# Kernel optimization log

Hardware: AMD Instinct MI355X
Metric: run time of the kernel (lower is better)

The kernel has to match this reference:

```python
import jax, jax.numpy as jnp
import numpy as np

N_NODES, D_H, D_MSG, N_LAYERS = 512, 64, 64, 3
T, E = 128, 8192


def setup_inputs() -> dict:
    key = jax.random.key(0)
    ks = jax.random.split(key, 16)
    s = 0.1
    t = jax.random.uniform(ks[0], (T,), dtype=jnp.float32)
    edge_index = jax.random.randint(ks[1], (2, E), 0, N_NODES, dtype=jnp.int64)
    inp = {
        "t": t,
        "edge_index": edge_index,
        "enc_w": jax.random.normal(ks[2], (1 + N_NODES, D_H), jnp.float32) * s,
        "enc_b": jnp.zeros((D_H,), jnp.float32),
        "msg1_w": jax.random.normal(ks[3], (N_LAYERS, 2 * D_H, D_MSG), jnp.float32) * s,
        "msg1_b": jnp.zeros((N_LAYERS, D_MSG), jnp.float32),
        "msg2_w": jax.random.normal(ks[4], (N_LAYERS, D_MSG, D_MSG), jnp.float32) * s,
        "msg2_b": jnp.zeros((N_LAYERS, D_MSG), jnp.float32),
        "upd1_w": jax.random.normal(ks[5], (N_LAYERS, D_H + D_MSG, D_H), jnp.float32) * s,
        "upd1_b": jnp.zeros((N_LAYERS, D_H), jnp.float32),
        "upd2_w": jax.random.normal(ks[6], (N_LAYERS, D_H, D_H), jnp.float32) * s,
        "upd2_b": jnp.zeros((N_LAYERS, D_H), jnp.float32),
        "ro_w": jax.random.normal(ks[7], (D_H, 1), jnp.float32) * s,
        "ro_b": jnp.zeros((1,), jnp.float32),
    }
    return inp


def reference(t, edge_index, enc_w, enc_b, msg1_w, msg1_b, msg2_w, msg2_b,
              upd1_w, upd1_b, upd2_w, upd2_b, ro_w, ro_b):
    Tn = t.shape[0]
    N = enc_w.shape[0] - 1
    L = msg1_w.shape[0]
    # node features: [t, one_hot(node_id)] -> encode
    t_feat = jnp.broadcast_to(t[:, None, None], (Tn, N, 1))          # [T,N,1]
    id_feat = jnp.broadcast_to(jnp.eye(N, dtype=t.dtype), (Tn, N, N))  # [T,N,N]
    x = jnp.concatenate([t_feat, id_feat], axis=-1)                   # [T,N,1+N]
    h = x @ enc_w + enc_b                                             # [T,N,d_h]
    src, dst = edge_index[0], edge_index[1]
    for l in range(L):
        # message MLP on gathered [h_src, h_dst]
        cat = jnp.concatenate([h[:, src], h[:, dst]], axis=-1)        # [T,E,2*d_h]
        m = jax.nn.silu(cat @ msg1_w[l] + msg1_b[l]) @ msg2_w[l] + msg2_b[l]  # [T,E,d_msg]
        # scatter-add into destination nodes (index_add)
        agg = jnp.zeros((Tn, N, m.shape[-1]), dtype=h.dtype).at[:, dst].add(m)
        u = jnp.concatenate([h, agg], axis=-1)                        # [T,N,d_h+d_msg]
        upd = jax.nn.silu(u @ upd1_w[l] + upd1_b[l]) @ upd2_w[l] + upd2_b[l]
        h = h + upd                                                   # residual
    out = (h @ ro_w + ro_b)[..., 0]                                   # [T,N]
    return out
```

## Files before the change

### kernel.cpp

```cpp
#include <hip/hip_runtime.h>

#define TT 128
#define NN 512
#define DH 64
#define EE 8192
#define LOB (18 * 8 * 64)

typedef __bf16 bf16x8 __attribute__((ext_vector_type(8)));
typedef float f32x4 __attribute__((ext_vector_type(4)));

struct US8 { unsigned short u[8]; };
struct Frag { bf16x8 hi, lo; };

static __device__ __forceinline__ unsigned short f2bf(float x) {
    union { float f; unsigned u; } c; c.f = x;
    unsigned r = (c.u + 0x7FFFu + ((c.u >> 16) & 1u)) >> 16;
    return (unsigned short)r;
}
static __device__ __forceinline__ float bf2f(unsigned short b) {
    union { unsigned u; float f; } c; c.u = ((unsigned)b) << 16;
    return c.f;
}
static __device__ __forceinline__ float silu_acc(float a, float b, float acc) {
    float x = a + b;
    float e = __expf(-x);
    return fmaf(x, __builtin_amdgcn_rcpf(1.0f + e), acc);
}
static __device__ __forceinline__ float silu_f(float x) {
    float e = __expf(-x);
    return x * __builtin_amdgcn_rcpf(1.0f + e);
}
static __device__ __forceinline__ Frag split8(const float* v) {
    Frag f;
    #pragma unroll
    for (int i = 0; i < 8; ++i) {
        __bf16 hb = (__bf16)v[i];
        f.hi[i] = hb;
        f.lo[i] = (__bf16)(v[i] - (float)hb);
    }
    return f;
}
static __device__ __forceinline__ f32x4 mmac(bf16x8 a, uint4 bw, f32x4 c) {
    return __builtin_amdgcn_mfma_f32_16x16x32_bf16(
        a, __builtin_bit_cast(bf16x8, bw), c, 0, 0, 0);
}
static __device__ __forceinline__ f32x4 mm3(Frag a, uint4 wh, uint4 wl, f32x4 c) {
    c = mmac(a.hi, wh, c);
    c = mmac(a.lo, wh, c);
    c = mmac(a.hi, wl, c);
    return c;
}

__global__ __launch_bounds__(512) void setup_kernel(
    const int* __restrict__ ei,
    const float* __restrict__ msg1_w, const float* __restrict__ msg2_w,
    const float* __restrict__ upd1_w, const float* __restrict__ upd2_w,
    const float* __restrict__ enc_w, const float* __restrict__ enc_b,
    const float* __restrict__ msg1_b,
    uint4* __restrict__ pack,
    int* __restrict__ counts, int* __restrict__ offsets,
    int* __restrict__ ssrc,
    float* __restrict__ E1s, float* __restrict__ E1d,
    float* __restrict__ e0sum) {
    int b = blockIdx.x;
    if (b < 18) {
        int l = b / 6, bi = b % 6;
        const float* W;
        if (bi == 0)      W = msg1_w + (size_t)l * 128 * 64;
        else if (bi == 1) W = msg1_w + (size_t)l * 128 * 64 + 64 * 64;
        else if (bi == 2) W = msg2_w + (size_t)l * 64 * 64;
        else if (bi == 3) W = upd1_w + (size_t)l * 128 * 64;
        else if (bi == 4) W = upd1_w + (size_t)l * 128 * 64 + 64 * 64;
        else              W = upd2_w + (size_t)l * 64 * 64;
        int lane = threadIdx.x & 63;
        int sub  = threadIdx.x >> 6;
        int nt = sub >> 1, kc = sub & 1;
        US8 oh, ol;
        #pragma unroll
        for (int i = 0; i < 8; ++i) {
            int k = kc * 32 + (lane >> 4) * 8 + i;
            int col = nt * 16 + (lane & 15);
            float w = W[k * 64 + col];
            unsigned short hu = f2bf(w);
            oh.u[i] = hu;
            ol.u[i] = f2bf(w - bf2f(hu));
        }
        size_t fi = ((size_t)b * 8 + sub) * 64 + lane;
        pack[fi]       = __builtin_bit_cast(uint4, oh);
        pack[LOB + fi] = __builtin_bit_cast(uint4, ol);
        return;
    }
    if (b == 18) {
        __shared__ int cnt[NN];
        __shared__ int tmp[NN];
        __shared__ int cur[NN];
        int i = threadIdx.x;
        cnt[i] = 0;
        __syncthreads();
        #pragma unroll
        for (int r = 0; r < EE / 512; ++r)
            atomicAdd(&cnt[ei[EE + r * 512 + i]], 1);
        __syncthreads();
        int c = cnt[i];
        tmp[i] = c;
        __syncthreads();
        for (int off = 1; off < NN; off <<= 1) {
            int v = (i >= off) ? tmp[i - off] : 0;
            __syncthreads();
            tmp[i] += v;
            __syncthreads();
        }
        counts[i] = c;
        offsets[i + 1] = tmp[i];
        if (i == 0) offsets[0] = 0;
        cur[i] = tmp[i] - c;
        __syncthreads();
        #pragma unroll
        for (int r = 0; r < EE / 512; ++r) {
            int e = r * 512 + i;
            int dst = ei[EE + e];
            int pos = atomicAdd(&cur[dst], 1);
            ssrc[pos] = ei[e];
        }
        return;
    }
    if (b < 83) {
        int nn = (b - 19) * 8 + (threadIdx.x >> 6);
        int d  = threadIdx.x & 63;
        float s = 0.f, dd = msg1_b[d];
        #pragma unroll 8
        for (int k = 0; k < 64; ++k) {
            float c = enc_w[(1 + nn) * 64 + k] + enc_b[k];
            s  = fmaf(c, msg1_w[k * 64 + d], s);
            dd = fmaf(c, msg1_w[(64 + k) * 64 + d], dd);
        }
        E1s[nn * 64 + d] = s;
        E1d[nn * 64 + d] = dd;
        return;
    }
    if (threadIdx.x < 64) {
        int d = threadIdx.x;
        float s = 0.f, dd = 0.f;
        #pragma unroll 8
        for (int k = 0; k < 64; ++k) {
            float a = enc_w[k];
            s  = fmaf(a, msg1_w[k * 64 + d], s);
            dd = fmaf(a, msg1_w[(64 + k) * 64 + d], dd);
        }
        e0sum[d] = s + dd;
    }
}

static __device__ __forceinline__ int swz_rowbase(int bid, int w) {
    int xcd = bid & 7;
    int idx = bid >> 3;
    int tt  = xcd * 16 + (idx >> 3);
    int sub = idx & 7;
    return tt * NN + sub * 64 + w * 16;
}

__global__ __launch_bounds__(256) void agg0_kernel(
    const float* __restrict__ t, const float* __restrict__ e0sum,
    const float* __restrict__ E1s, const float* __restrict__ E1d,
    const int* __restrict__ offsets, const int* __restrict__ ssrc,
    float* __restrict__ aggpre) {
    int bid = blockIdx.x;
    int xcd = bid & 7;
    int idx = bid >> 3;
    int tt  = xcd * 16 + (idx >> 7);
    int n   = (idx & 127) * 4 + (threadIdx.x >> 6);
    int lane = threadIdx.x & 63;
    int eg = lane >> 4;
    int chb = (lane & 15) * 4;
    int ch4 = chb * 4;
    float tv = t[tt];
    float4 e0 = *(const float4*)(e0sum + chb);
    float4 ed = *(const float4*)(E1d + n * DH + chb);
    float4 base = make_float4(fmaf(tv, e0.x, ed.x), fmaf(tv, e0.y, ed.y),
                              fmaf(tv, e0.z, ed.z), fmaf(tv, e0.w, ed.w));
    int beg = offsets[n], end = offsets[n + 1];
    const char* Eb = (const char*)E1s;
    float4 acc = make_float4(0.f, 0.f, 0.f, 0.f);
    int i = beg + eg;
    for (; i + 4 < end; i += 8) {
        int s0 = ssrc[i] << 8;
        int s1 = ssrc[i + 4] << 8;
        float4 v0 = *(const float4*)(Eb + s0 + ch4);
        float4 v1 = *(const float4*)(Eb + s1 + ch4);
        acc.x = silu_acc(v0.x, base.x, acc.x);
        acc.y = silu_acc(v0.y, base.y, acc.y);
        acc.z = silu_acc(v0.z, base.z, acc.z);
        acc.w = silu_acc(v0.w, base.w, acc.w);
        acc.x = silu_acc(v1.x, base.x, acc.x);
        acc.y = silu_acc(v1.y, base.y, acc.y);
        acc.z = silu_acc(v1.z, base.z, acc.z);
        acc.w = silu_acc(v1.w, base.w, acc.w);
    }
    if (i < end) {
        int s0 = ssrc[i] << 8;
        float4 v0 = *(const float4*)(Eb + s0 + ch4);
        acc.x = silu_acc(v0.x, base.x, acc.x);
        acc.y = silu_acc(v0.y, base.y, acc.y);
        acc.z = silu_acc(v0.z, base.z, acc.z);
        acc.w = silu_acc(v0.w, base.w, acc.w);
    }
    acc.x += __shfl_xor(acc.x, 16); acc.x += __shfl_xor(acc.x, 32);
    acc.y += __shfl_xor(acc.y, 16); acc.y += __shfl_xor(acc.y, 32);
    acc.z += __shfl_xor(acc.z, 16); acc.z += __shfl_xor(acc.z, 32);
    acc.w += __shfl_xor(acc.w, 16); acc.w += __shfl_xor(acc.w, 32);
    if (eg == 0)
        *(float4*)(aggpre + ((size_t)tt * NN + n) * DH + chb) = acc;
}

__global__ __launch_bounds__(256) void agg_kernel(
    const float* __restrict__ hs, const float* __restrict__ hd,
    const int* __restrict__ offsets, const int* __restrict__ ssrc,
    float* __restrict__ aggpre) {
    int bid = blockIdx.x;
    int xcd = bid & 7;
    int idx = bid >> 3;
    int tt  = xcd * 16 + (idx >> 7);
    int n   = (idx & 127) * 4 + (threadIdx.x >> 6);
    int lane = threadIdx.x & 63;
    size_t rowoff = ((size_t)tt * NN + n) * DH;
    int eg = lane >> 4;
    int ch4 = (lane & 15) * 16;
    float4 hdv = *(const float4*)(hd + rowoff + (lane & 15) * 4);
    int beg = offsets[n], end = offsets[n + 1];
    const char* hb = (const char*)(hs + (size_t)tt * NN * DH);
    float4 acc = make_float4(0.f, 0.f, 0.f, 0.f);
    int i = beg + eg;
    for (; i + 4 < end; i += 8) {
        int s0 = ssrc[i] << 8;
        int s1 = ssrc[i + 4] << 8;
        float4 v0 = *(const float4*)(hb + s0 + ch4);
        float4 v1 = *(const float4*)(hb + s1 + ch4);
        acc.x = silu_acc(v0.x, hdv.x, acc.x);
        acc.y = silu_acc(v0.y, hdv.y, acc.y);
        acc.z = silu_acc(v0.z, hdv.z, acc.z);
        acc.w = silu_acc(v0.w, hdv.w, acc.w);
        acc.x = silu_acc(v1.x, hdv.x, acc.x);
        acc.y = silu_acc(v1.y, hdv.y, acc.y);
        acc.z = silu_acc(v1.z, hdv.z, acc.z);
        acc.w = silu_acc(v1.w, hdv.w, acc.w);
    }
    if (i < end) {
        int s0 = ssrc[i] << 8;
        float4 v0 = *(const float4*)(hb + s0 + ch4);
        acc.x = silu_acc(v0.x, hdv.x, acc.x);
        acc.y = silu_acc(v0.y, hdv.y, acc.y);
        acc.z = silu_acc(v0.z, hdv.z, acc.z);
        acc.w = silu_acc(v0.w, hdv.w, acc.w);
    }
    acc.x += __shfl_xor(acc.x, 16); acc.x += __shfl_xor(acc.x, 32);
    acc.y += __shfl_xor(acc.y, 16); acc.y += __shfl_xor(acc.y, 32);
    acc.z += __shfl_xor(acc.z, 16); acc.z += __shfl_xor(acc.z, 32);
    acc.w += __shfl_xor(acc.w, 16); acc.w += __shfl_xor(acc.w, 32);
    if (eg == 0) *(float4*)(aggpre + rowoff + (lane & 15) * 4) = acc;
}

__global__ __launch_bounds__(256) void upd_mfma_kernel(
    float* __restrict__ h, const float* __restrict__ aggpre,
    const float* __restrict__ t, const float* __restrict__ enc_w,
    const float* __restrict__ enc_b,
    const int* __restrict__ counts, const uint4* __restrict__ pack, int l,
    const float* __restrict__ b2, const float* __restrict__ ub1,
    const float* __restrict__ ub2, const float* __restrict__ b1n,
    float* __restrict__ hs, float* __restrict__ hd,
    const float* __restrict__ ro_w, const float* __restrict__ ro_b,
    float* __restrict__ out, int first, int last) {
    __shared__ float tile[4][16 * 68];
    int lane = threadIdx.x & 63;
    int w = threadIdx.x >> 6;
    int rowbase = swz_rowbase(blockIdx.x, w);
    float* TA = tile[w];
    int arow = lane & 15, kgrp = lane >> 4, k0 = kgrp * 8;
    int hrow = rowbase + arow;

    float hf[16];
    if (first) {
        int n = (rowbase & (NN - 1)) + arow;
        float tv = t[rowbase >> 9];
        #pragma unroll
        for (int kc = 0; kc < 2; ++kc)
            #pragma unroll
            for (int i = 0; i < 8; ++i) {
                int k = kc * 32 + k0 + i;
                hf[kc * 8 + i] = tv * enc_w[k] + enc_w[(1 + n) * DH + k] + enc_b[k];
            }
    } else {
        *(float4*)&hf[0]  = *(const float4*)(h + (size_t)hrow * DH + k0);
        *(float4*)&hf[4]  = *(const float4*)(h + (size_t)hrow * DH + k0 + 4);
        *(float4*)&hf[8]  = *(const float4*)(h + (size_t)hrow * DH + 32 + k0);
        *(float4*)&hf[12] = *(const float4*)(h + (size_t)hrow * DH + 32 + k0 + 4);
    }
    Frag ha0 = split8(&hf[0]), ha1 = split8(&hf[8]);

    float gf[16];
    *(float4*)&gf[0]  = *(const float4*)(aggpre + (size_t)hrow * DH + k0);
    *(float4*)&gf[4]  = *(const float4*)(aggpre + (size_t)hrow * DH + k0 + 4);
    *(float4*)&gf[8]  = *(const float4*)(aggpre + (size_t)hrow * DH + 32 + k0);
    *(float4*)&gf[12] = *(const float4*)(aggpre + (size_t)hrow * DH + 32 + k0 + 4);
    Frag ga0 = split8(&gf[0]), ga1 = split8(&gf[8]);

    const uint4* PW2H = pack + (size_t)(l * 6 + 2) * 512;
    const uint4* PW2L = PW2H + LOB;
    float degv[4];
    #pragma unroll
    for (int r = 0; r < 4; ++r)
        degv[r] = (float)counts[(rowbase + kgrp * 4 + r) & (NN - 1)];
    #pragma unroll
    for (int nt = 0; nt < 4; ++nt) {
        float b2v = b2[nt * 16 + (lane & 15)];
        f32x4 a;
        #pragma unroll
        for (int r = 0; r < 4; ++r) a[r] = degv[r] * b2v;
        a = mm3(ga0, PW2H[(nt * 2 + 0) * 64 + lane], PW2L[(nt * 2 + 0) * 64 + lane], a);
        a = mm3(ga1, PW2H[(nt * 2 + 1) * 64 + lane], PW2L[(nt * 2 + 1) * 64 + lane], a);
        #pragma unroll
        for (int r = 0; r < 4; ++r)
            TA[(kgrp * 4 + r) * 68 + nt * 16 + (lane & 15)] = a[r];
    }
    float za[16];
    #pragma unroll
    for (int i = 0; i < 8; ++i) za[i] = TA[arow * 68 + k0 + i];
    #pragma unroll
    for (int i = 0; i < 8; ++i) za[8 + i] = TA[arow * 68 + 32 + k0 + i];
    Frag ka0 = split8(&za[0]), ka1 = split8(&za[8]);

    const uint4* PU1tH = pack + (size_t)(l * 6 + 3) * 512;
    const uint4* PU1bH = pack + (size_t)(l * 6 + 4) * 512;
    const uint4* PU1tL = PU1tH + LOB;
    const uint4* PU1bL = PU1bH + LOB;
    #pragma unroll
    for (int nt = 0; nt < 4; ++nt) {
        float bv = ub1[nt * 16 + (lane & 15)];
        f32x4 a;
        #pragma unroll
        for (int r = 0; r < 4; ++r) a[r] = bv;
        a = mm3(ha0, PU1tH[(nt * 2 + 0) * 64 + lane], PU1tL[(nt * 2 + 0) * 64 + lane], a);
        a = mm3(ha1, PU1tH[(nt * 2 + 1) * 64 + lane], PU1tL[(nt * 2 + 1) * 64 + lane], a);
        a = mm3(ka0, PU1bH[(nt * 2 + 0) * 64 + lane], PU1bL[(nt * 2 + 0) * 64 + lane], a);
        a = mm3(ka1, PU1bH[(nt * 2 + 1) * 64 + lane], PU1bL[(nt * 2 + 1) * 64 + lane], a);
        #pragma unroll
        for (int r = 0; r < 4; ++r)
            TA[(kgrp * 4 + r) * 68 + nt * 16 + (lane & 15)] = silu_f(a[r]);
    }
    float zb[16];
    #pragma unroll
    for (int i = 0; i < 8; ++i) zb[i] = TA[arow * 68 + k0 + i];
    #pragma unroll
    for (int i = 0; i < 8; ++i) zb[8 + i] = TA[arow * 68 + 32 + k0 + i];
    Frag kz0 = split8(&zb[0]), kz1 = split8(&zb[8]);

    const uint4* PU2H = pack + (size_t)(l * 6 + 5) * 512;
    const uint4* PU2L = PU2H + LOB;
    #pragma unroll
    for (int nt = 0; nt < 4; ++nt) {
        float bv = ub2[nt * 16 + (lane & 15)];
        f32x4 a;
        #pragma unroll
        for (int r = 0; r < 4; ++r) a[r] = bv;
        a = mm3(kz0, PU2H[(nt * 2 + 0) * 64 + lane], PU2L[(nt * 2 + 0) * 64 + lane], a);
        a = mm3(kz1, PU2H[(nt * 2 + 1) * 64 + lane], PU2L[(nt * 2 + 1) * 64 + lane], a);
        #pragma unroll
        for (int r = 0; r < 4; ++r)
            TA[(kgrp * 4 + r) * 68 + nt * 16 + (lane & 15)] = a[r];
    }
    float hn[16];
    #pragma unroll
    for (int i = 0; i < 8; ++i) hn[i] = hf[i] + TA[arow * 68 + k0 + i];
    #pragma unroll
    for (int i = 0; i < 8; ++i) hn[8 + i] = hf[8 + i] + TA[arow * 68 + 32 + k0 + i];

    if (last) {
        float v = 0.f;
        #pragma unroll
        for (int i = 0; i < 8; ++i) v += hn[i] * ro_w[k0 + i];
        #pragma unroll
        for (int i = 0; i < 8; ++i) v += hn[8 + i] * ro_w[32 + k0 + i];
        v += __shfl_xor(v, 16);
        v += __shfl_xor(v, 32);
        if (lane < 16) out[rowbase + lane] = v + ro_b[0];
        return;
    }

    *(float4*)(h + (size_t)hrow * DH + k0) = make_float4(hn[0], hn[1], hn[2], hn[3]);
    *(float4*)(h + (size_t)hrow * DH + k0 + 4) = make_float4(hn[4], hn[5], hn[6], hn[7]);
    *(float4*)(h + (size_t)hrow * DH + 32 + k0) = make_float4(hn[8], hn[9], hn[10], hn[11]);
    *(float4*)(h + (size_t)hrow * DH + 32 + k0 + 4) = make_float4(hn[12], hn[13], hn[14], hn[15]);

    Frag na0 = split8(&hn[0]), na1 = split8(&hn[8]);
    const uint4* PWtH = pack + (size_t)((l + 1) * 6 + 0) * 512;
    const uint4* PWbH = pack + (size_t)((l + 1) * 6 + 1) * 512;
    const uint4* PWtL = PWtH + LOB;
    const uint4* PWbL = PWbH + LOB;
    #pragma unroll
    for (int nt = 0; nt < 4; ++nt) {
        f32x4 s; f32x4 d;
        float b1v = b1n[nt * 16 + (lane & 15)];
        #pragma unroll
        for (int r = 0; r < 4; ++r) { s[r] = 0.f; d[r] = b1v; }
        s = mm3(na0, PWtH[(nt * 2 + 0) * 64 + lane], PWtL[(nt * 2 + 0) * 64 + lane], s);
        s = mm3(na1, PWtH[(nt * 2 + 1) * 64 + lane], PWtL[(nt * 2 + 1) * 64 + lane], s);
        d = mm3(na0, PWbH[(nt * 2 + 0) * 64 + lane], PWbL[(nt * 2 + 0) * 64 + lane], d);
        d = mm3(na1, PWbH[(nt * 2 + 1) * 64 + lane], PWbL[(nt * 2 + 1) * 64 + lane], d);
        #pragma unroll
        for (int r = 0; r < 4; ++r) {
            int rr = rowbase + kgrp * 4 + r;
            hs[(size_t)rr * DH + nt * 16 + (lane & 15)] = s[r];
            hd[(size_t)rr * DH + nt * 16 + (lane & 15)] = d[r];
        }
    }
}

extern "C" void kernel_launch(void* const* d_in, const int* in_sizes, int n_in,
                              void* d_out, int out_size, void* d_ws, size_t ws_size,
                              hipStream_t stream) {
    const float* t      = (const float*)d_in[0];
    const int*   ei     = (const int*)d_in[1];
    const float* enc_w  = (const float*)d_in[2];
    const float* enc_b  = (const float*)d_in[3];
    const float* msg1_w = (const float*)d_in[4];
    const float* msg1_b = (const float*)d_in[5];
    const float* msg2_w = (const float*)d_in[6];
    const float* msg2_b = (const float*)d_in[7];
    const float* upd1_w = (const float*)d_in[8];
    const float* upd1_b = (const float*)d_in[9];
    const float* upd2_w = (const float*)d_in[10];
    const float* upd2_b = (const float*)d_in[11];
    const float* ro_w   = (const float*)d_in[12];
    const float* ro_b   = (const float*)d_in[13];
    float* out = (float*)d_out;

    const size_t HN = (size_t)TT * NN * DH;
    float* h      = (float*)d_ws;
    float* hs     = h + HN;
    float* hd     = hs + HN;
    float* aggpre = hd + HN;
    uint4* pack   = (uint4*)(aggpre + HN);
    int* counts  = (int*)(pack + 2 * LOB);
    int* offsets = counts + NN;
    int* ssrc    = offsets + NN + 1;
    float* E1s   = (float*)(ssrc + EE);
    float* E1d   = E1s + NN * DH;
    float* e0sum = E1d + NN * DH;

    setup_kernel<<<84, 512, 0, stream>>>(ei, msg1_w, msg2_w, upd1_w, upd2_w,
                                         enc_w, enc_b, msg1_b,
                                         pack, counts, offsets, ssrc,
                                         E1s, E1d, e0sum);

    for (int l = 0; l < 3; ++l) {
        if (l == 0)
            agg0_kernel<<<TT * NN / 4, 256, 0, stream>>>(
                t, e0sum, E1s, E1d, offsets, ssrc, aggpre);
        else
            agg_kernel<<<TT * NN / 4, 256, 0, stream>>>(
                hs, hd, offsets, ssrc, aggpre);
        int last = (l == 2);
        upd_mfma_kernel<<<TT * NN / 64, 256, 0, stream>>>(
            h, aggpre, t, enc_w, enc_b, counts, pack, l,
            msg2_b + (size_t)l * DH, upd1_b + (size_t)l * DH,
            upd2_b + (size_t)l * DH,
            last ? msg1_b : msg1_b + (size_t)(l + 1) * DH,
            hs, hd, ro_w, ro_b, out, (l == 0) ? 1 : 0, last);
    }
}
```

Before: 247.2 us.

## Fuse edge aggregation and node update MLP into one per-layer kernel

Merges the gather/aggregate kernel and the MFMA update kernel into a single layer kernel in which each block of 16 node rows aggregates incoming messages into shared memory and then runs the update and next-layer projection MLPs. This removes the aggpre round trip through global memory and halves kernel launches per layer. The hs buffer is double-buffered because other blocks still read the previous layer's hs while this one writes. Each block now handles 16 rows instead of 64, and warps split output columns with more __syncthreads. This can lower MFMA efficiency and lengthen per-block serial latency.

```diff
diff --git a/kernel.cpp b/kernel.cpp
--- a/kernel.cpp
+++ b/kernel.cpp
@@ -151,265 +151,207 @@
     }
 }
 
-static __device__ __forceinline__ int swz_rowbase(int bid, int w) {
-    int xcd = bid & 7;
-    int idx = bid >> 3;
-    int tt  = xcd * 16 + (idx >> 3);
-    int sub = idx & 7;
-    return tt * NN + sub * 64 + w * 16;
-}
-
-__global__ __launch_bounds__(256) void agg0_kernel(
-    const float* __restrict__ t, const float* __restrict__ e0sum,
+__global__ __launch_bounds__(256) void layer_kernel(
+    const float* __restrict__ t, const float* __restrict__ enc_w,
+    const float* __restrict__ enc_b, const float* __restrict__ e0sum,
     const float* __restrict__ E1s, const float* __restrict__ E1d,
-    const int* __restrict__ offsets, const int* __restrict__ ssrc,
-    float* __restrict__ aggpre) {
+    float* __restrict__ h, const float* __restrict__ hs_in,
+    float* __restrict__ hs_out, float* __restrict__ hd,
+    const int* __restrict__ counts, const int* __restrict__ offsets,
+    const int* __restrict__ ssrc, const uint4* __restrict__ pack, int l,
+    const float* __restrict__ b2, const float* __restrict__ ub1,
+    const float* __restrict__ ub2, const float* __restrict__ b1n,
+    const float* __restrict__ ro_w, const float* __restrict__ ro_b,
+    float* __restrict__ out, int first, int last) {
+    __shared__ float AG[16 * 68];
+    __shared__ float HH[16 * 68];
+    __shared__ float ST[16 * 68];
+    int lane = threadIdx.x & 63;
+    int w = threadIdx.x >> 6;
     int bid = blockIdx.x;
     int xcd = bid & 7;
     int idx = bid >> 3;
-    int tt  = xcd * 16 + (idx >> 7);
-    int n   = (idx & 127) * 4 + (threadIdx.x >> 6);
-    int lane = threadIdx.x & 63;
-    int eg = lane >> 4;
-    int chb = (lane & 15) * 4;
-    int ch4 = chb * 4;
+    int tt  = xcd * 16 + (idx >> 5);
+    int grp = idx & 31;
+    int rowbase = tt * NN + grp * 16;
+    int nbase = grp * 16;
+    int arow = lane & 15, kgrp = lane >> 4, k0 = kgrp * 8;
     float tv = t[tt];
-    float4 e0 = *(const float4*)(e0sum + chb);
-    float4 ed = *(const float4*)(E1d + n * DH + chb);
-    float4 base = make_float4(fmaf(tv, e0.x, ed.x), fmaf(tv, e0.y, ed.y),
-                              fmaf(tv, e0.z, ed.z), fmaf(tv, e0.w, ed.w));
-    int beg = offsets[n], end = offsets[n + 1];
-    const char* Eb = (const char*)E1s;
-    float4 acc = make_float4(0.f, 0.f, 0.f, 0.f);
-    int i = beg + eg;
-    for (; i + 4 < end; i += 8) {
-        int s0 = ssrc[i] << 8;
-        int s1 = ssrc[i + 4] << 8;
-        float4 v0 = *(const float4*)(Eb + s0 + ch4);
-        float4 v1 = *(const float4*)(Eb + s1 + ch4);
-        acc.x = silu_acc(v0.x, base.x, acc.x);
-        acc.y = silu_acc(v0.y, base.y, acc.y);
-        acc.z = silu_acc(v0.z, base.z, acc.z);
-        acc.w = silu_acc(v0.w, base.w, acc.w);
-        acc.x = silu_acc(v1.x, base.x, acc.x);
-        acc.y = silu_acc(v1.y, base.y, acc.y);
-        acc.z = silu_acc(v1.z, base.z, acc.z);
-        acc.w = silu_acc(v1.w, base.w, acc.w);
-    }
-    if (i < end) {
-        int s0 = ssrc[i] << 8;
-        float4 v0 = *(const float4*)(Eb + s0 + ch4);
-        acc.x = silu_acc(v0.x, base.x, acc.x);
-        acc.y = silu_acc(v0.y, base.y, acc.y);
-        acc.z = silu_acc(v0.z, base.z, acc.z);
-        acc.w = silu_acc(v0.w, base.w, acc.w);
-    }
-    acc.x += __shfl_xor(acc.x, 16); acc.x += __shfl_xor(acc.x, 32);
-    acc.y += __shfl_xor(acc.y, 16); acc.y += __shfl_xor(acc.y, 32);
-    acc.z += __shfl_xor(acc.z, 16); acc.z += __shfl_xor(acc.z, 32);
-    acc.w += __shfl_xor(acc.w, 16); acc.w += __shfl_xor(acc.w, 32);
-    if (eg == 0)
-        *(float4*)(aggpre + ((size_t)tt * NN + n) * DH + chb) = acc;
-}
-
-__global__ __launch_bounds__(256) void agg_kernel(
-    const float* __restrict__ hs, const float* __restrict__ hd,
-    const int* __restrict__ offsets, const int* __restrict__ ssrc,
-    float* __restrict__ aggpre) {
-    int bid = blockIdx.x;
-    int xcd = bid & 7;
-    int idx = bid >> 3;
-    int tt  = xcd * 16 + (idx >> 7);
-    int n   = (idx & 127) * 4 + (threadIdx.x >> 6);
-    int lane = threadIdx.x & 63;
-    size_t rowoff = ((size_t)tt * NN + n) * DH;
-    int eg = lane >> 4;
-    int ch4 = (lane & 15) * 16;
-    float4 hdv = *(const float4*)(hd + rowoff + (lane & 15) * 4);
-    int beg = offsets[n], end = offsets[n + 1];
-    const char* hb = (const char*)(hs + (size_t)tt * NN * DH);
-    float4 acc = make_float4(0.f, 0.f, 0.f, 0.f);
-    int i = beg + eg;
-    for (; i + 4 < end; i += 8) {
-        int s0 = ssrc[i] << 8;
-        int s1 = ssrc[i + 4] << 8;
-        float4 v0 = *(const float4*)(hb + s0 + ch4);
-        float4 v1 = *(const float4*)(hb + s1 + ch4);
-        acc.x = silu_acc(v0.x, hdv.x, acc.x);
-        acc.y = silu_acc(v0.y, hdv.y, acc.y);
-        acc.z = silu_acc(v0.z, hdv.z, acc.z);
-        acc.w = silu_acc(v0.w, hdv.w, acc.w);
-        acc.x = silu_acc(v1.x, hdv.x, acc.x);
-        acc.y = silu_acc(v1.y, hdv.y, acc.y);
-        acc.z = silu_acc(v1.z, hdv.z, acc.z);
-        acc.w = silu_acc(v1.w, hdv.w, acc.w);
-    }
-    if (i < end) {
-        int s0 = ssrc[i] << 8;
-        float4 v0 = *(const float4*)(hb + s0 + ch4);
-        acc.x = silu_acc(v0.x, hdv.x, acc.x);
-        acc.y = silu_acc(v0.y, hdv.y, acc.y);
-        acc.z = silu_acc(v0.z, hdv.z, acc.z);
-        acc.w = silu_acc(v0.w, hdv.w, acc.w);
-    }
-    acc.x += __shfl_xor(acc.x, 16); acc.x += __shfl_xor(acc.x, 32);
-    acc.y += __shfl_xor(acc.y, 16); acc.y += __shfl_xor(acc.y, 32);
-    acc.z += __shfl_xor(acc.z, 16); acc.z += __shfl_xor(acc.z, 32);
-    acc.w += __shfl_xor(acc.w, 16); acc.w += __shfl_xor(acc.w, 32);
-    if (eg == 0) *(float4*)(aggpre + rowoff + (lane & 15) * 4) = acc;
-}
-
-__global__ __launch_bounds__(256) void upd_mfma_kernel(
-    float* __restrict__ h, const float* __restrict__ aggpre,
-    const float* __restrict__ t, const float* __restrict__ enc_w,
-    const float* __restrict__ enc_b,
-    const int* __restrict__ counts, const uint4* __restrict__ pack, int l,
-    const float* __restrict__ b2, const float* __restrict__ ub1,
-    const float* __restrict__ ub2, const float* __restrict__ b1n,
-    float* __restrict__ hs, float* __restrict__ hd,
-    const float* __restrict__ ro_w, const float* __restrict__ ro_b,
-    float* __restrict__ out, int first, int last) {
-    __shared__ float tile[4][16 * 68];
-    int lane = threadIdx.x & 63;
-    int w = threadIdx.x >> 6;
-    int rowbase = swz_rowbase(blockIdx.x, w);
-    float* TA = tile[w];
-    int arow = lane & 15, kgrp = lane >> 4, k0 = kgrp * 8;
-    int hrow = rowbase + arow;
-
-    float hf[16];
-    if (first) {
-        int n = (rowbase & (NN - 1)) + arow;
-        float tv = t[rowbase >> 9];
-        #pragma unroll
-        for (int kc = 0; kc < 2; ++kc)
-            #pragma unroll
-            for (int i = 0; i < 8; ++i) {
-                int k = kc * 32 + k0 + i;
-                hf[kc * 8 + i] = tv * enc_w[k] + enc_w[(1 + n) * DH + k] + enc_b[k];
+
+    {
+        int eg = lane >> 4;
+        int chb = (lane & 15) * 4;
+        int ch4 = chb * 4;
+        const char* gb = first ? (const char*)E1s
+                               : (const char*)(hs_in + (size_t)tt * NN * DH);
+        for (int j = w * 4; j < w * 4 + 4; ++j) {
+            int nn = nbase + j;
+            float4 base;
+            if (first) {
+                float4 e0 = *(const float4*)(e0sum + chb);
+                float4 ed = *(const float4*)(E1d + nn * DH + chb);
+                base = make_float4(fmaf(tv, e0.x, ed.x), fmaf(tv, e0.y, ed.y),
+                                   fmaf(tv, e0.z, ed.z), fmaf(tv, e0.w, ed.w));
+            } else {
+                base = *(const float4*)(hd + ((size_t)tt * NN + nn) * DH + chb);
             }
-    } else {
-        *(float4*)&hf[0]  = *(const float4*)(h + (size_t)hrow * DH + k0);
-        *(float4*)&hf[4]  = *(const float4*)(h + (size_t)hrow * DH + k0 + 4);
-        *(float4*)&hf[8]  = *(const float4*)(h + (size_t)hrow * DH + 32 + k0);
-        *(float4*)&hf[12] = *(const float4*)(h + (size_t)hrow * DH + 32 + k0 + 4);
-    }
-    Frag ha0 = split8(&hf[0]), ha1 = split8(&hf[8]);
-
-    float gf[16];
-    *(float4*)&gf[0]  = *(const float4*)(aggpre + (size_t)hrow * DH + k0);
-    *(float4*)&gf[4]  = *(const float4*)(aggpre + (size_t)hrow * DH + k0 + 4);
-    *(float4*)&gf[8]  = *(const float4*)(aggpre + (size_t)hrow * DH + 32 + k0);
-    *(float4*)&gf[12] = *(const float4*)(aggpre + (size_t)hrow * DH + 32 + k0 + 4);
-    Frag ga0 = split8(&gf[0]), ga1 = split8(&gf[8]);
-
-    const uint4* PW2H = pack + (size_t)(l * 6 + 2) * 512;
-    const uint4* PW2L = PW2H + LOB;
-    float degv[4];
-    #pragma unroll
-    for (int r = 0; r < 4; ++r)
-        degv[r] = (float)counts[(rowbase + kgrp * 4 + r) & (NN - 1)];
-    #pragma unroll
-    for (int nt = 0; nt < 4; ++nt) {
-        float b2v = b2[nt * 16 + (lane & 15)];
+            int beg = offsets[nn], end = offsets[nn + 1];
+            float4 acc = make_float4(0.f, 0.f, 0.f, 0.f);
+            int i = beg + eg;
+            for (; i + 4 < end; i += 8) {
+                int s0 = ssrc[i] << 8;
+                int s1 = ssrc[i + 4] << 8;
+                float4 v0 = *(const float4*)(gb + s0 + ch4);
+                float4 v1 = *(const float4*)(gb + s1 + ch4);
+                acc.x = silu_acc(v0.x, base.x, acc.x);
+                acc.y = silu_acc(v0.y, base.y, acc.y);
+                acc.z = silu_acc(v0.z, base.z, acc.z);
+                acc.w = silu_acc(v0.w, base.w, acc.w);
+                acc.x = silu_acc(v1.x, base.x, acc.x);
+                acc.y = silu_acc(v1.y, base.y, acc.y);
+                acc.z = silu_acc(v1.z, base.z, acc.z);
+                acc.w = silu_acc(v1.w, base.w, acc.w);
+            }
+            if (i < end) {
+                int s0 = ssrc[i] << 8;
+                float4 v0 = *(const float4*)(gb + s0 + ch4);
+                acc.x = silu_acc(v0.x, base.x, acc.x);
+                acc.y = silu_acc(v0.y, base.y, acc.y);
+                acc.z = silu_acc(v0.z, base.z, acc.z);
+                acc.w = silu_acc(v0.w, base.w, acc.w);
+            }
+            acc.x += __shfl_xor(acc.x, 16); acc.x += __shfl_xor(acc.x, 32);
+            acc.y += __shfl_xor(acc.y, 16); acc.y += __shfl_xor(acc.y, 32);
+            acc.z += __shfl_xor(acc.z, 16); acc.z += __shfl_xor(acc.z, 32);
+            acc.w += __shfl_xor(acc.w, 16); acc.w += __shfl_xor(acc.w, 32);
+            if (eg == 0) *(float4*)(&AG[j * 68 + chb]) = acc;
+        }
+        if (first) {
+            for (int j = w * 4; j < w * 4 + 4; ++j) {
+                int nn = nbase + j;
+                HH[j * 68 + lane] =
+                    tv * enc_w[lane] + enc_w[(1 + nn) * DH + lane] + enc_b[lane];
+            }
+        } else {
+            for (int j = w * 4; j < w * 4 + 4; ++j)
+                HH[j * 68 + lane] = h[((size_t)rowbase + j) * DH + lane];
+        }
+    }
+    __syncthreads();
+
+    {
+        float za[16];
+        #pragma unroll
+        for (int i = 0; i < 8; ++i) za[i] = AG[arow * 68 + k0 + i];
+        #pragma unroll
+        for (int i = 0; i < 8; ++i) za[8 + i] = AG[arow * 68 + 32 + k0 + i];
+        Frag ga0 = split8(&za[0]), ga1 = split8(&za[8]);
+        const uint4* PW2H = pack + (size_t)(l * 6 + 2) * 512;
+        const uint4* PW2L = PW2H + LOB;
+        float b2v = b2[w * 16 + (lane & 15)];
         f32x4 a;
         #pragma unroll
-        for (int r = 0; r < 4; ++r) a[r] = degv[r] * b2v;
-        a = mm3(ga0, PW2H[(nt * 2 + 0) * 64 + lane], PW2L[(nt * 2 + 0) * 64 + lane], a);
-        a = mm3(ga1, PW2H[(nt * 2 + 1) * 64 + lane], PW2L[(nt * 2 + 1) * 64 + lane], a);
-        #pragma unroll
         for (int r = 0; r < 4; ++r)
-            TA[(kgrp * 4 + r) * 68 + nt * 16 + (lane & 15)] = a[r];
-    }
-    float za[16];
-    #pragma unroll
-    for (int i = 0; i < 8; ++i) za[i] = TA[arow * 68 + k0 + i];
-    #pragma unroll
-    for (int i = 0; i < 8; ++i) za[8 + i] = TA[arow * 68 + 32 + k0 + i];
-    Frag ka0 = split8(&za[0]), ka1 = split8(&za[8]);
-
-    const uint4* PU1tH = pack + (size_t)(l * 6 + 3) * 512;
-    const uint4* PU1bH = pack + (size_t)(l * 6 + 4) * 512;
-    const uint4* PU1tL = PU1tH + LOB;
-    const uint4* PU1bL = PU1bH + LOB;
-    #pragma unroll
-    for (int nt = 0; nt < 4; ++nt) {
-        float bv = ub1[nt * 16 + (lane & 15)];
+            a[r] = (float)counts[nbase + kgrp * 4 + r] * b2v;
+        a = mm3(ga0, PW2H[(w * 2 + 0) * 64 + lane], PW2L[(w * 2 + 0) * 64 + lane], a);
+        a = mm3(ga1, PW2H[(w * 2 + 1) * 64 + lane], PW2L[(w * 2 + 1) * 64 + lane], a);
+        #pragma unroll
+        for (int r = 0; r < 4; ++r)
+            ST[(kgrp * 4 + r) * 68 + w * 16 + (lane & 15)] = a[r];
+    }
+    __syncthreads();
+
+    {
+        float hf[16];
+        #pragma unroll
+        for (int i = 0; i < 8; ++i) hf[i] = HH[arow * 68 + k0 + i];
+        #pragma unroll
+        for (int i = 0; i < 8; ++i) hf[8 + i] = HH[arow * 68 + 32 + k0 + i];
+        Frag ha0 = split8(&hf[0]), ha1 = split8(&hf[8]);
+        float ka[16];
+        #pragma unroll
+        for (int i = 0; i < 8; ++i) ka[i] = ST[arow * 68 + k0 + i];
+        #pragma unroll
+        for (int i = 0; i < 8; ++i) ka[8 + i] = ST[arow * 68 + 32 + k0 + i];
+        Frag ka0 = split8(&ka[0]), ka1 = split8(&ka[8]);
+        const uint4* PU1tH = pack + (size_t)(l * 6 + 3) * 512;
+        const uint4* PU1bH = pack + (size_t)(l * 6 + 4) * 512;
+        const uint4* PU1tL = PU1tH + LOB;
+        const uint4* PU1bL = PU1bH + LOB;
+        float bv = ub1[w * 16 + (lane & 15)];
         f32x4 a;
         #pragma unroll
         for (int r = 0; r < 4; ++r) a[r] = bv;
-        a = mm3(ha0, PU1tH[(nt * 2 + 0) * 64 + lane], PU1tL[(nt * 2 + 0) * 64 + lane], a);
-        a = mm3(ha1, PU1tH[(nt * 2 + 1) * 64 + lane], PU1tL[(nt * 2 + 1) * 64 + lane], a);
-        a = mm3(ka0, PU1bH[(nt * 2 + 0) * 64 + lane], PU1bL[(nt * 2 + 0) * 64 + lane], a);
-        a = mm3(ka1, PU1bH[(nt * 2 + 1) * 64 + lane], PU1bL[(nt * 2 + 1) * 64 + lane], a);
+        a = mm3(ha0, PU1tH[(w * 2 + 0) * 64 + lane], PU1tL[(w * 2 + 0) * 64 + lane], a);
+        a = mm3(ha1, PU1tH[(w * 2 + 1) * 64 + lane], PU1tL[(w * 2 + 1) * 64 + lane], a);
+        a = mm3(ka0, PU1bH[(w * 2 + 0) * 64 + lane], PU1bL[(w * 2 + 0) * 64 + lane], a);
+        a = mm3(ka1, PU1bH[(w * 2 + 1) * 64 + lane], PU1bL[(w * 2 + 1) * 64 + lane], a);
+        __syncthreads();
         #pragma unroll
         for (int r = 0; r < 4; ++r)
-            TA[(kgrp * 4 + r) * 68 + nt * 16 + (lane & 15)] = silu_f(a[r]);
-    }
-    float zb[16];
-    #pragma unroll
-    for (int i = 0; i < 8; ++i) zb[i] = TA[arow * 68 + k0 + i];
-    #pragma unroll
-    for (int i = 0; i < 8; ++i) zb[8 + i] = TA[arow * 68 + 32 + k0 + i];
-    Frag kz0 = split8(&zb[0]), kz1 = split8(&zb[8]);
-
-    const uint4* PU2H = pack + (size_t)(l * 6 + 5) * 512;
-    const uint4* PU2L = PU2H + LOB;
-    #pragma unroll
-    for (int nt = 0; nt < 4; ++nt) {
-        float bv = ub2[nt * 16 + (lane & 15)];
+            AG[(kgrp * 4 + r) * 68 + w * 16 + (lane & 15)] = silu_f(a[r]);
+    }
+    __syncthreads();
+
+    {
+        float kz[16];
+        #pragma unroll
+        for (int i = 0; i < 8; ++i) kz[i] = AG[arow * 68 + k0 + i];
+        #pragma unroll
+        for (int i = 0; i < 8; ++i) kz[8 + i] = AG[arow * 68 + 32 + k0 + i];
+        Frag kz0 = split8(&kz[0]), kz1 = split8(&kz[8]);
+        const uint4* PU2H = pack + (size_t)(l * 6 + 5) * 512;
+        const uint4* PU2L = PU2H + LOB;
+        float bv = ub2[w * 16 + (lane & 15)];
         f32x4 a;
         #pragma unroll
         for (int r = 0; r < 4; ++r) a[r] = bv;
-        a = mm3(kz0, PU2H[(nt * 2 + 0) * 64 + lane], PU2L[(nt * 2 + 0) * 64 + lane], a);
-        a = mm3(kz1, PU2H[(nt * 2 + 1) * 64 + lane], PU2L[(nt * 2 + 1) * 64 + lane], a);
+        a = mm3(kz0, PU2H[(w * 2 + 0) * 64 + lane], PU2L[(w * 2 + 0) * 64 + lane], a);
+        a = mm3(kz1, PU2H[(w * 2 + 1) * 64 + lane], PU2L[(w * 2 + 1) * 64 + lane], a);
         #pragma unroll
         for (int r = 0; r < 4; ++r)
-            TA[(kgrp * 4 + r) * 68 + nt * 16 + (lane & 15)] = a[r];
-    }
-    float hn[16];
-    #pragma unroll
-    for (int i = 0; i < 8; ++i) hn[i] = hf[i] + TA[arow * 68 + k0 + i];
-    #pragma unroll
-    for (int i = 0; i < 8; ++i) hn[8 + i] = hf[8 + i] + TA[arow * 68 + 32 + k0 + i];
+            HH[(kgrp * 4 + r) * 68 + w * 16 + (lane & 15)] += a[r];
+    }
+    __syncthreads();
 
     if (last) {
-        float v = 0.f;
-        #pragma unroll
-        for (int i = 0; i < 8; ++i) v += hn[i] * ro_w[k0 + i];
-        #pragma unroll
-        for (int i = 0; i < 8; ++i) v += hn[8 + i] * ro_w[32 + k0 + i];
-        v += __shfl_xor(v, 16);
-        v += __shfl_xor(v, 32);
-        if (lane < 16) out[rowbase + lane] = v + ro_b[0];
+        #pragma unroll
+        for (int r = 0; r < 4; ++r) {
+            int j = w * 4 + r;
+            float v = HH[j * 68 + lane] * ro_w[lane];
+            v += __shfl_xor(v, 1);  v += __shfl_xor(v, 2);
+            v += __shfl_xor(v, 4);  v += __shfl_xor(v, 8);
+            v += __shfl_xor(v, 16); v += __shfl_xor(v, 32);
+            if (lane == 0) out[rowbase + j] = v + ro_b[0];
+        }
         return;
     }
-
-    *(float4*)(h + (size_t)hrow * DH + k0) = make_float4(hn[0], hn[1], hn[2], hn[3]);
-    *(float4*)(h + (size_t)hrow * DH + k0 + 4) = make_float4(hn[4], hn[5], hn[6], hn[7]);
-    *(float4*)(h + (size_t)hrow * DH + 32 + k0) = make_float4(hn[8], hn[9], hn[10], hn[11]);
-    *(float4*)(h + (size_t)hrow * DH + 32 + k0 + 4) = make_float4(hn[12], hn[13], hn[14], hn[15]);
-
-    Frag na0 = split8(&hn[0]), na1 = split8(&hn[8]);
-    const uint4* PWtH = pack + (size_t)((l + 1) * 6 + 0) * 512;
-    const uint4* PWbH = pack + (size_t)((l + 1) * 6 + 1) * 512;
-    const uint4* PWtL = PWtH + LOB;
-    const uint4* PWbL = PWbH + LOB;
-    #pragma unroll
-    for (int nt = 0; nt < 4; ++nt) {
+    for (int j = w * 4; j < w * 4 + 4; ++j)
+        h[((size_t)rowbase + j) * DH + lane] = HH[j * 68 + lane];
+    {
+        float hn[16];
+        #pragma unroll
+        for (int i = 0; i < 8; ++i) hn[i] = HH[arow * 68 + k0 + i];
+        #pragma unroll
+        for (int i = 0; i < 8; ++i) hn[8 + i] = HH[arow * 68 + 32 + k0 + i];
+        Frag na0 = split8(&hn[0]), na1 = split8(&hn[8]);
+        const uint4* PWtH = pack + (size_t)((l + 1) * 6 + 0) * 512;
+        const uint4* PWbH = pack + (size_t)((l + 1) * 6 + 1) * 512;
+        const uint4* PWtL = PWtH + LOB;
+        const uint4* PWbL = PWbH + LOB;
+        float b1v = b1n[w * 16 + (lane & 15)];
         f32x4 s; f32x4 d;
-        float b1v = b1n[nt * 16 + (lane & 15)];
         #pragma unroll
         for (int r = 0; r < 4; ++r) { s[r] = 0.f; d[r] = b1v; }
-        s = mm3(na0, PWtH[(nt * 2 + 0) * 64 + lane], PWtL[(nt * 2 + 0) * 64 + lane], s);
-        s = mm3(na1, PWtH[(nt * 2 + 1) * 64 + lane], PWtL[(nt * 2 + 1) * 64 + lane], s);
-        d = mm3(na0, PWbH[(nt * 2 + 0) * 64 + lane], PWbL[(nt * 2 + 0) * 64 + lane], d);
-        d = mm3(na1, PWbH[(nt * 2 + 1) * 64 + lane], PWbL[(nt * 2 + 1) * 64 + lane], d);
+        s = mm3(na0, PWtH[(w * 2 + 0) * 64 + lane], PWtL[(w * 2 + 0) * 64 + lane], s);
+        s = mm3(na1, PWtH[(w * 2 + 1) * 64 + lane], PWtL[(w * 2 + 1) * 64 + lane], s);
+        d = mm3(na0, PWbH[(w * 2 + 0) * 64 + lane], PWbL[(w * 2 + 0) * 64 + lane], d);
+        d = mm3(na1, PWbH[(w * 2 + 1) * 64 + lane], PWbL[(w * 2 + 1) * 64 + lane], d);
         #pragma unroll
         for (int r = 0; r < 4; ++r) {
             int rr = rowbase + kgrp * 4 + r;
-            hs[(size_t)rr * DH + nt * 16 + (lane & 15)] = s[r];
-            hd[(size_t)rr * DH + nt * 16 + (lane & 15)] = d[r];
+            hs_out[(size_t)rr * DH + w * 16 + (lane & 15)] = s[r];
+            hd[(size_t)rr * DH + w * 16 + (lane & 15)] = d[r];
         }
     }
 }
@@ -434,11 +376,11 @@
     float* out = (float*)d_out;
 
     const size_t HN = (size_t)TT * NN * DH;
-    float* h      = (float*)d_ws;
-    float* hs     = h + HN;
-    float* hd     = hs + HN;
-    float* aggpre = hd + HN;
-    uint4* pack   = (uint4*)(aggpre + HN);
+    float* h    = (float*)d_ws;
+    float* hs0  = h + HN;
+    float* hs1  = hs0 + HN;
+    float* hd   = hs1 + HN;
+    uint4* pack = (uint4*)(hd + HN);
     int* counts  = (int*)(pack + 2 * LOB);
     int* offsets = counts + NN;
     int* ssrc    = offsets + NN + 1;
@@ -452,18 +394,16 @@
                                          E1s, E1d, e0sum);
 
     for (int l = 0; l < 3; ++l) {
-        if (l == 0)
-            agg0_kernel<<<TT * NN / 4, 256, 0, stream>>>(
-                t, e0sum, E1s, E1d, offsets, ssrc, aggpre);
-        else
-            agg_kernel<<<TT * NN / 4, 256, 0, stream>>>(
-                hs, hd, offsets, ssrc, aggpre);
-        int last = (l == 2);
-        upd_mfma_kernel<<<TT * NN / 64, 256, 0, stream>>>(
-            h, aggpre, t, enc_w, enc_b, counts, pack, l,
+        int first = (l == 0), last = (l == 2);
+        const float* hs_in = (l == 1) ? hs0 : hs1;
+        float* hs_out      = (l == 0) ? hs0 : hs1;
+        layer_kernel<<<TT * NN / 16, 256, 0, stream>>>(
+            t, enc_w, enc_b, e0sum, E1s, E1d,
+            h, hs_in, hs_out, hd,
+            counts, offsets, ssrc, pack, l,
             msg2_b + (size_t)l * DH, upd1_b + (size_t)l * DH,
             upd2_b + (size_t)l * DH,
             last ? msg1_b : msg1_b + (size_t)(l + 1) * DH,
-            hs, hd, ro_w, ro_b, out, (l == 0) ? 1 : 0, last);
-    }
-}
+            ro_w, ro_b, out, first, last);
+    }
+}
```

Measured after the change: 258.3 us. 1.04x slower.

## Fold msg2 weights into upd1 bottom half and unroll aggregation gather

Applied to the files above, without the earlier changes.

Precomputes G = msg2_w · upd1_w_bottom and c2 = msg2_b · upd1_w_bottom in the setup kernel, so the update kernel applies the aggregated pre-activation directly through one fused weight. This removes one 64x64 split-bf16 MFMA stage and an LDS round trip per layer. Both aggregation kernels are also moved onto a shared macro whose gather loop is unrolled to four edges per iteration, giving more loads in flight. The folded product is computed in fp32 and then split into hi/lo bf16, which slightly changes rounding.

```diff
diff --git a/kernel.cpp b/kernel.cpp
--- a/kernel.cpp
+++ b/kernel.cpp
@@ -55,23 +55,49 @@
     const int* __restrict__ ei,
     const float* __restrict__ msg1_w, const float* __restrict__ msg2_w,
     const float* __restrict__ upd1_w, const float* __restrict__ upd2_w,
+    const float* __restrict__ msg2_b,
     const float* __restrict__ enc_w, const float* __restrict__ enc_b,
     const float* __restrict__ msg1_b,
     uint4* __restrict__ pack,
     int* __restrict__ counts, int* __restrict__ offsets,
     int* __restrict__ ssrc,
     float* __restrict__ E1s, float* __restrict__ E1d,
-    float* __restrict__ e0sum) {
+    float* __restrict__ e0sum, float* __restrict__ c2) {
     int b = blockIdx.x;
     if (b < 18) {
         int l = b / 6, bi = b % 6;
         const float* W;
         if (bi == 0)      W = msg1_w + (size_t)l * 128 * 64;
         else if (bi == 1) W = msg1_w + (size_t)l * 128 * 64 + 64 * 64;
-        else if (bi == 2) W = msg2_w + (size_t)l * 64 * 64;
         else if (bi == 3) W = upd1_w + (size_t)l * 128 * 64;
         else if (bi == 4) W = upd1_w + (size_t)l * 128 * 64 + 64 * 64;
-        else              W = upd2_w + (size_t)l * 64 * 64;
+        else if (bi == 5) W = upd2_w + (size_t)l * 64 * 64;
+        else              W = nullptr;
+        __shared__ float Gs[64 * 64];
+        if (bi == 2) {
+            const float* W2  = msg2_w + (size_t)l * 64 * 64;
+            const float* U1b = upd1_w + (size_t)l * 128 * 64 + 64 * 64;
+            int k = threadIdx.x >> 3;
+            int dbase = (threadIdx.x & 7) * 8;
+            float acc[8] = {0.f, 0.f, 0.f, 0.f, 0.f, 0.f, 0.f, 0.f};
+            for (int j = 0; j < 64; ++j) {
+                float a = W2[k * 64 + j];
+                #pragma unroll
+                for (int i = 0; i < 8; ++i)
+                    acc[i] = fmaf(a, U1b[j * 64 + dbase + i], acc[i]);
+            }
+            #pragma unroll
+            for (int i = 0; i < 8; ++i) Gs[k * 64 + dbase + i] = acc[i];
+            if (threadIdx.x < 64) {
+                int d = threadIdx.x;
+                float s = 0.f;
+                for (int j = 0; j < 64; ++j)
+                    s = fmaf(msg2_b[l * 64 + j], U1b[j * 64 + d], s);
+                c2[l * 64 + d] = s;
+            }
+            __syncthreads();
+            W = Gs;
+        }
         int lane = threadIdx.x & 63;
         int sub  = threadIdx.x >> 6;
         int nt = sub >> 1, kc = sub & 1;
@@ -158,6 +184,62 @@
     int sub = idx & 7;
     return tt * NN + sub * 64 + w * 16;
 }
+
+#define AGG_BODY(GB, BASE)                                                     \
+    float4 acc = make_float4(0.f, 0.f, 0.f, 0.f);                              \
+    int i = beg + eg;                                                          \
+    for (; i + 12 < end; i += 16) {                                            \
+        int s0 = ssrc[i] << 8;                                                 \
+        int s1 = ssrc[i + 4] << 8;                                             \
+        int s2 = ssrc[i + 8] << 8;                                             \
+        int s3 = ssrc[i + 12] << 8;                                            \
+        float4 v0 = *(const float4*)(GB + s0 + ch4);                           \
+        float4 v1 = *(const float4*)(GB + s1 + ch4);                           \
+        float4 v2 = *(const float4*)(GB + s2 + ch4);                           \
+        float4 v3 = *(const float4*)(GB + s3 + ch4);                           \
+        acc.x = silu_acc(v0.x, BASE.x, acc.x);                                 \
+        acc.y = silu_acc(v0.y, BASE.y, acc.y);                                 \
+        acc.z = silu_acc(v0.z, BASE.z, acc.z);                                 \
+        acc.w = silu_acc(v0.w, BASE.w, acc.w);                                 \
+        acc.x = silu_acc(v1.x, BASE.x, acc.x);                                 \
+        acc.y = silu_acc(v1.y, BASE.y, acc.y);                                 \
+        acc.z = silu_acc(v1.z, BASE.z, acc.z);                                 \
+        acc.w = silu_acc(v1.w, BASE.w, acc.w);                                 \
+        acc.x = silu_acc(v2.x, BASE.x, acc.x);                                 \
+        acc.y = silu_acc(v2.y, BASE.y, acc.y);                                 \
+        acc.z = silu_acc(v2.z, BASE.z, acc.z);                                 \
+        acc.w = silu_acc(v2.w, BASE.w, acc.w);                                 \
+        acc.x = silu_acc(v3.x, BASE.x, acc.x);                                 \
+        acc.y = silu_acc(v3.y, BASE.y, acc.y);                                 \
+        acc.z = silu_acc(v3.z, BASE.z, acc.z);                                 \
+        acc.w = silu_acc(v3.w, BASE.w, acc.w);                                 \
+    }                                                                          \
+    for (; i + 4 < end; i += 8) {                                              \
+        int s0 = ssrc[i] << 8;                                                 \
+        int s1 = ssrc[i + 4] << 8;                                             \
+        float4 v0 = *(const float4*)(GB + s0 + ch4);                           \
+        float4 v1 = *(const float4*)(GB + s1 + ch4);                           \
+        acc.x = silu_acc(v0.x, BASE.x, acc.x);                                 \
+        acc.y = silu_acc(v0.y, BASE.y, acc.y);                                 \
+        acc.z = silu_acc(v0.z, BASE.z, acc.z);                                 \
+        acc.w = silu_acc(v0.w, BASE.w, acc.w);                                 \
+        acc.x = silu_acc(v1.x, BASE.x, acc.x);                                 \
+        acc.y = silu_acc(v1.y, BASE.y, acc.y);                                 \
+        acc.z = silu_acc(v1.z, BASE.z, acc.z);                                 \
+        acc.w = silu_acc(v1.w, BASE.w, acc.w);                                 \
+    }                                                                          \
+    if (i < end) {                                                             \
+        int s0 = ssrc[i] << 8;                                                 \
+        float4 v0 = *(const float4*)(GB + s0 + ch4);                           \
+        acc.x = silu_acc(v0.x, BASE.x, acc.x);                                 \
+        acc.y = silu_acc(v0.y, BASE.y, acc.y);                                 \
+        acc.z = silu_acc(v0.z, BASE.z, acc.z);                                 \
+        acc.w = silu_acc(v0.w, BASE.w, acc.w);                                 \
+    }                                                                          \
+    acc.x += __shfl_xor(acc.x, 16); acc.x += __shfl_xor(acc.x, 32);            \
+    acc.y += __shfl_xor(acc.y, 16); acc.y += __shfl_xor(acc.y, 32);            \
+    acc.z += __shfl_xor(acc.z, 16); acc.z += __shfl_xor(acc.z, 32);            \
+    acc.w += __shfl_xor(acc.w, 16); acc.w += __shfl_xor(acc.w, 32);
 
 __global__ __launch_bounds__(256) void agg0_kernel(
     const float* __restrict__ t, const float* __restrict__ e0sum,
@@ -180,34 +262,7 @@
                               fmaf(tv, e0.z, ed.z), fmaf(tv, e0.w, ed.w));
     int beg = offsets[n], end = offsets[n + 1];
     const char* Eb = (const char*)E1s;
-    float4 acc = make_float4(0.f, 0.f, 0.f, 0.f);
-    int i = beg + eg;
-    for (; i + 4 < end; i += 8) {
-        int s0 = ssrc[i] << 8;
-        int s1 = ssrc[i + 4] << 8;
-        float4 v0 = *(const float4*)(Eb + s0 + ch4);
-        float4 v1 = *(const float4*)(Eb + s1 + ch4);
-        acc.x = silu_acc(v0.x, base.x, acc.x);
-        acc.y = silu_acc(v0.y, base.y, acc.y);
-        acc.z = silu_acc(v0.z, base.z, acc.z);
-        acc.w = silu_acc(v0.w, base.w, acc.w);
-        acc.x = silu_acc(v1.x, base.x, acc.x);
-        acc.y = silu_acc(v1.y, base.y, acc.y);
-        acc.z = silu_acc(v1.z, base.z, acc.z);
-        acc.w = silu_acc(v1.w, base.w, acc.w);
-    }
-    if (i < end) {
-        int s0 = ssrc[i] << 8;
-        float4 v0 = *(const float4*)(Eb + s0 + ch4);
-        acc.x = silu_acc(v0.x, base.x, acc.x);
-        acc.y = silu_acc(v0.y, base.y, acc.y);
-        acc.z = silu_acc(v0.z, base.z, acc.z);
-        acc.w = silu_acc(v0.w, base.w, acc.w);
-    }
-    acc.x += __shfl_xor(acc.x, 16); acc.x += __shfl_xor(acc.x, 32);
-    acc.y += __shfl_xor(acc.y, 16); acc.y += __shfl_xor(acc.y, 32);
-    acc.z += __shfl_xor(acc.z, 16); acc.z += __shfl_xor(acc.z, 32);
-    acc.w += __shfl_xor(acc.w, 16); acc.w += __shfl_xor(acc.w, 32);
+    AGG_BODY(Eb, base)
     if (eg == 0)
         *(float4*)(aggpre + ((size_t)tt * NN + n) * DH + chb) = acc;
 }
@@ -224,39 +279,13 @@
     int lane = threadIdx.x & 63;
     size_t rowoff = ((size_t)tt * NN + n) * DH;
     int eg = lane >> 4;
-    int ch4 = (lane & 15) * 16;
-    float4 hdv = *(const float4*)(hd + rowoff + (lane & 15) * 4);
+    int chb = (lane & 15) * 4;
+    int ch4 = chb * 4;
+    float4 hdv = *(const float4*)(hd + rowoff + chb);
     int beg = offsets[n], end = offsets[n + 1];
     const char* hb = (const char*)(hs + (size_t)tt * NN * DH);
-    float4 acc = make_float4(0.f, 0.f, 0.f, 0.f);
-    int i = beg + eg;
-    for (; i + 4 < end; i += 8) {
-        int s0 = ssrc[i] << 8;
-        int s1 = ssrc[i + 4] << 8;
-        float4 v0 = *(const float4*)(hb + s0 + ch4);
-        float4 v1 = *(const float4*)(hb + s1 + ch4);
-        acc.x = silu_acc(v0.x, hdv.x, acc.x);
-        acc.y = silu_acc(v0.y, hdv.y, acc.y);
-        acc.z = silu_acc(v0.z, hdv.z, acc.z);
-        acc.w = silu_acc(v0.w, hdv.w, acc.w);
-        acc.x = silu_acc(v1.x, hdv.x, acc.x);
-        acc.y = silu_acc(v1.y, hdv.y, acc.y);
-        acc.z = silu_acc(v1.z, hdv.z, acc.z);
-        acc.w = silu_acc(v1.w, hdv.w, acc.w);
-    }
-    if (i < end) {
-        int s0 = ssrc[i] << 8;
-        float4 v0 = *(const float4*)(hb + s0 + ch4);
-        acc.x = silu_acc(v0.x, hdv.x, acc.x);
-        acc.y = silu_acc(v0.y, hdv.y, acc.y);
-        acc.z = silu_acc(v0.z, hdv.z, acc.z);
-        acc.w = silu_acc(v0.w, hdv.w, acc.w);
-    }
-    acc.x += __shfl_xor(acc.x, 16); acc.x += __shfl_xor(acc.x, 32);
-    acc.y += __shfl_xor(acc.y, 16); acc.y += __shfl_xor(acc.y, 32);
-    acc.z += __shfl_xor(acc.z, 16); acc.z += __shfl_xor(acc.z, 32);
-    acc.w += __shfl_xor(acc.w, 16); acc.w += __shfl_xor(acc.w, 32);
-    if (eg == 0) *(float4*)(aggpre + rowoff + (lane & 15) * 4) = acc;
+    AGG_BODY(hb, hdv)
+    if (eg == 0) *(float4*)(aggpre + rowoff + chb) = acc;
 }
 
 __global__ __launch_bounds__(256) void upd_mfma_kernel(
@@ -264,7 +293,7 @@
     const float* __restrict__ t, const float* __restrict__ enc_w,
     const float* __restrict__ enc_b,
     const int* __restrict__ counts, const uint4* __restrict__ pack, int l,
-    const float* __restrict__ b2, const float* __restrict__ ub1,
+    const float* __restrict__ c2, const float* __restrict__ ub1,
     const float* __restrict__ ub2, const float* __restrict__ b1n,
     float* __restrict__ hs, float* __restrict__ hd,
     const float* __restrict__ ro_w, const float* __restrict__ ro_b,
@@ -303,45 +332,26 @@
     *(float4*)&gf[12] = *(const float4*)(aggpre + (size_t)hrow * DH + 32 + k0 + 4);
     Frag ga0 = split8(&gf[0]), ga1 = split8(&gf[8]);
 
-    const uint4* PW2H = pack + (size_t)(l * 6 + 2) * 512;
-    const uint4* PW2L = PW2H + LOB;
+    const uint4* PGH  = pack + (size_t)(l * 6 + 2) * 512;
+    const uint4* PGL  = PGH + LOB;
+    const uint4* PU1tH = pack + (size_t)(l * 6 + 3) * 512;
+    const uint4* PU1tL = PU1tH + LOB;
+    const float* c2l = c2 + l * 64;
     float degv[4];
     #pragma unroll
     for (int r = 0; r < 4; ++r)
         degv[r] = (float)counts[(rowbase + kgrp * 4 + r) & (NN - 1)];
     #pragma unroll
     for (int nt = 0; nt < 4; ++nt) {
-        float b2v = b2[nt * 16 + (lane & 15)];
+        float bv  = ub1[nt * 16 + (lane & 15)];
+        float c2v = c2l[nt * 16 + (lane & 15)];
         f32x4 a;
         #pragma unroll
-        for (int r = 0; r < 4; ++r) a[r] = degv[r] * b2v;
-        a = mm3(ga0, PW2H[(nt * 2 + 0) * 64 + lane], PW2L[(nt * 2 + 0) * 64 + lane], a);
-        a = mm3(ga1, PW2H[(nt * 2 + 1) * 64 + lane], PW2L[(nt * 2 + 1) * 64 + lane], a);
-        #pragma unroll
-        for (int r = 0; r < 4; ++r)
-            TA[(kgrp * 4 + r) * 68 + nt * 16 + (lane & 15)] = a[r];
-    }
-    float za[16];
-    #pragma unroll
-    for (int i = 0; i < 8; ++i) za[i] = TA[arow * 68 + k0 + i];
-    #pragma unroll
-    for (int i = 0; i < 8; ++i) za[8 + i] = TA[arow * 68 + 32 + k0 + i];
-    Frag ka0 = split8(&za[0]), ka1 = split8(&za[8]);
-
-    const uint4* PU1tH = pack + (size_t)(l * 6 + 3) * 512;
-    const uint4* PU1bH = pack + (size_t)(l * 6 + 4) * 512;
-    const uint4* PU1tL = PU1tH + LOB;
-    const uint4* PU1bL = PU1bH + LOB;
-    #pragma unroll
-    for (int nt = 0; nt < 4; ++nt) {
-        float bv = ub1[nt * 16 + (lane & 15)];
-        f32x4 a;
-        #pragma unroll
-        for (int r = 0; r < 4; ++r) a[r] = bv;
+        for (int r = 0; r < 4; ++r) a[r] = fmaf(degv[r], c2v, bv);
         a = mm3(ha0, PU1tH[(nt * 2 + 0) * 64 + lane], PU1tL[(nt * 2 + 0) * 64 + lane], a);
         a = mm3(ha1, PU1tH[(nt * 2 + 1) * 64 + lane], PU1tL[(nt * 2 + 1) * 64 + lane], a);
-        a = mm3(ka0, PU1bH[(nt * 2 + 0) * 64 + lane], PU1bL[(nt * 2 + 0) * 64 + lane], a);
-        a = mm3(ka1, PU1bH[(nt * 2 + 1) * 64 + lane], PU1bL[(nt * 2 + 1) * 64 + lane], a);
+        a = mm3(ga0, PGH[(nt * 2 + 0) * 64 + lane], PGL[(nt * 2 + 0) * 64 + lane], a);
+        a = mm3(ga1, PGH[(nt * 2 + 1) * 64 + lane], PGL[(nt * 2 + 1) * 64 + lane], a);
         #pragma unroll
         for (int r = 0; r < 4; ++r)
             TA[(kgrp * 4 + r) * 68 + nt * 16 + (lane & 15)] = silu_f(a[r]);
@@ -445,11 +455,12 @@
     float* E1s   = (float*)(ssrc + EE);
     float* E1d   = E1s + NN * DH;
     float* e0sum = E1d + NN * DH;
+    float* c2    = e0sum + DH;
 
     setup_kernel<<<84, 512, 0, stream>>>(ei, msg1_w, msg2_w, upd1_w, upd2_w,
-                                         enc_w, enc_b, msg1_b,
+                                         msg2_b, enc_w, enc_b, msg1_b,
                                          pack, counts, offsets, ssrc,
-                                         E1s, E1d, e0sum);
+                                         E1s, E1d, e0sum, c2);
 
     for (int l = 0; l < 3; ++l) {
         if (l == 0)
@@ -461,7 +472,7 @@
         int last = (l == 2);
         upd_mfma_kernel<<<TT * NN / 64, 256, 0, stream>>>(
             h, aggpre, t, enc_w, enc_b, counts, pack, l,
-            msg2_b + (size_t)l * DH, upd1_b + (size_t)l * DH,
+            c2, upd1_b + (size_t)l * DH,
             upd2_b + (size_t)l * DH,
             last ? msg1_b : msg1_b + (size_t)(l + 1) * DH,
             hs, hd, ro_w, ro_b, out, (l == 0) ? 1 : 0, last);
```

Result: slower. 271.2 us (+9.7%).
